# Kernel optimization log

Hardware: AMD Instinct MI355X
Metric: run time of the kernel (lower is better)

The kernel has to match this reference:

```python
import jax, jax.numpy as jnp
import numpy as np

ALPHA = 0.2  # LeakyReLU slope
BN_EPS = 1e-5


def _conv_circ(x, w, b, pad_w):
    # circular padding only on width (torch padding=(0, pad_w), padding_mode='circular')
    x = jnp.pad(x, ((0, 0), (0, 0), (0, 0), (pad_w, pad_w)), mode='wrap')
    y = jax.lax.conv_general_dilated(x, w, window_strides=(1, 1), padding='VALID',
                                     dimension_numbers=('NCHW', 'OIHW', 'NCHW'))
    return y + b[None, :, None, None]


def _graph_conv(x, n, w, b, pad_w):
    h1 = _conv_circ(x, w, b, pad_w)  # [B, N, C, F]
    h2 = _conv_circ(n, w, b, pad_w)
    B, N, C, F = h1.shape
    h1f = h1.reshape(B, N, C * F)
    h2f = h2.reshape(B, N, C * F)
    a = jnp.einsum('bnf,bmf->bnm', h1f, h2f)          # [B, N, N]
    a = jnp.where(a > 0, a, ALPHA * a)                 # LeakyReLU
    att = jax.nn.softmax(a, axis=1)                    # torch Softmax(dim=1)
    return (att @ h1f).reshape(B, N, C, F)


def _bn_pool_relu(x, gamma, beta, mean, var):
    # eval-mode BatchNorm2d -> MaxPool2d((1,2)) -> ReLU
    inv = gamma / jnp.sqrt(var + BN_EPS)
    x = x * inv[None, :, None, None] + (beta - mean * inv)[None, :, None, None]
    W = x.shape[-1]
    W2 = (W // 2) * 2
    x = x[..., :W2].reshape(*x.shape[:-1], W2 // 2, 2).max(axis=-1)
    return jax.nn.relu(x)


def setup_inputs() -> dict:
    key = jax.random.key(0)
    ks = jax.random.split(key, 16)
    B = 16384
    return {
        'x': jax.random.normal(ks[0], (B, 5, 5, 50), jnp.float32),
        'conv1_w': jax.random.normal(ks[1], (32, 5, 5, 11), jnp.float32) * 0.1,
        'conv1_b': jax.random.normal(ks[2], (32,), jnp.float32) * 0.1,
        'bn1_gamma': jax.random.uniform(ks[3], (32,), jnp.float32, 0.5, 1.5),
        'bn1_beta': jax.random.normal(ks[4], (32,), jnp.float32) * 0.1,
        'bn1_mean': jax.random.normal(ks[5], (32,), jnp.float32) * 0.1,
        'bn1_var': jax.random.uniform(ks[6], (32,), jnp.float32, 0.5, 1.5),
        'conv2_w': jax.random.normal(ks[7], (32, 32, 1, 5), jnp.float32) * 0.1,
        'conv2_b': jax.random.normal(ks[8], (32,), jnp.float32) * 0.1,
        'bn2_gamma': jax.random.uniform(ks[9], (32,), jnp.float32, 0.5, 1.5),
        'bn2_beta': jax.random.normal(ks[10], (32,), jnp.float32) * 0.1,
        'bn2_mean': jax.random.normal(ks[11], (32,), jnp.float32) * 0.1,
        'bn2_var': jax.random.uniform(ks[12], (32,), jnp.float32, 0.5, 1.5),
        'lin_w': jax.random.normal(ks[13], (13, 384), jnp.float32) * 0.05,
        'lin_b': jax.random.normal(ks[14], (13,), jnp.float32) * 0.05,
    }


def reference(x, conv1_w, conv1_b, bn1_gamma, bn1_beta, bn1_mean, bn1_var,
              conv2_w, conv2_b, bn2_gamma, bn2_beta, bn2_mean, bn2_var,
              lin_w, lin_b):
    W = x.shape[-1]
    xa, na = x[..., :W // 2], x[..., W // 2:]
    xa = _graph_conv(xa, xa, conv1_w, conv1_b, 5)
    na = _graph_conv(na, na, conv1_w, conv1_b, 5)
    xa = _bn_pool_relu(xa, bn1_gamma, bn1_beta, bn1_mean, bn1_var)
    na = _bn_pool_relu(na, bn1_gamma, bn1_beta, bn1_mean, bn1_var)
    x2 = _graph_conv(xa, na, conv2_w, conv2_b, 2)
    n2 = _graph_conv(na, xa, conv2_w, conv2_b, 2)
    x2 = _bn_pool_relu(x2, bn2_gamma, bn2_beta, bn2_mean, bn2_var)
    n2 = _bn_pool_relu(n2, bn2_gamma, bn2_beta, bn2_mean, bn2_var)
    flat = jnp.concatenate([x2, n2], axis=-1).reshape(x.shape[0], -1)  # [B, 384]
    # Dropout(0.2) is identity in eval mode
    return flat @ lin_w.T + lin_b
```

## Files before the change

### kernel.cpp

```cpp
#include <hip/hip_runtime.h>
#include <math.h>

#define ALPHA 0.2f
#define BN_EPS 1e-5f

typedef __attribute__((ext_vector_type(8))) short short8;
typedef __attribute__((ext_vector_type(4))) float v4f;

__device__ __forceinline__ unsigned short f2bf_rne(float f) {
    union { float f; unsigned u; } x; x.f = f;
    unsigned r = x.u + 0x7FFFu + ((x.u >> 16) & 1u);
    return (unsigned short)(r >> 16);
}
__device__ __forceinline__ float bf2f(unsigned short h) {
    union { float f; unsigned u; } x; x.u = ((unsigned)h) << 16;
    return x.f;
}

__global__ __launch_bounds__(256) void prep_kernel(const float* __restrict__ w1,
                                                   const float* __restrict__ w2,
                                                   unsigned short* __restrict__ ws16) {
    int s = blockIdx.x * 256 + threadIdx.x;
    if (s < 1664) {
        int lane = s & 63;
        int ktnt = s >> 6;
        int Kt = ktnt % 13;
        int Nt = ktnt / 13;
        int oc = Nt * 16 + (lane & 15);
        int quad = lane >> 4;
        for (int j = 0; j < 8; ++j) {
            int kp = Kt * 32 + quad * 8 + j;
            int kw = kp & 15, ickh = kp >> 4;
            float w = 0.f;
            if (kw < 11 && ickh < 25) w = w1[oc * 275 + ickh * 11 + kw];
            unsigned short h = f2bf_rne(w);
            ws16[s * 8 + j] = h;
            ws16[13312 + s * 8 + j] = f2bf_rne(w - bf2f(h));
        }
    } else if (s < 2304) {
        int s2 = s - 1664;
        int lane = s2 & 63;
        int ktnt = s2 >> 6;
        int kw = ktnt >> 1;
        int nt = ktnt & 1;
        int oc = nt * 16 + (lane & 15);
        int quad = lane >> 4;
        for (int j = 0; j < 8; ++j) {
            int ic = quad * 8 + j;
            float w = w2[oc * 160 + ic * 5 + kw];
            unsigned short h = f2bf_rne(w);
            ws16[26624 + s2 * 8 + j] = h;
            ws16[31744 + s2 * 8 + j] = f2bf_rne(w - bf2f(h));
        }
    }
}

#define IT 4648
#define ATO 2112
#define P2O 4224
#define CSTO 9296
#define LDS_TOTAL (9296 + 128)
#define ABF_PER_IT 1844

__global__ __launch_bounds__(256, 4) void gcn_kernel(
    const float* __restrict__ x,
    const float* __restrict__ w1, const float* __restrict__ b1,
    const float* __restrict__ g1, const float* __restrict__ be1,
    const float* __restrict__ mu1, const float* __restrict__ va1,
    const float* __restrict__ w2, const float* __restrict__ b2,
    const float* __restrict__ g2, const float* __restrict__ be2,
    const float* __restrict__ mu2, const float* __restrict__ va2,
    const float* __restrict__ lw, const float* __restrict__ lb,
    const unsigned short* __restrict__ ws16,
    float* __restrict__ out)
{
    __shared__ float lds[LDS_TOTAL];
    float* cst = lds + CSTO;

    const int tid = threadIdx.x;
    const int b0  = blockIdx.x * 2;

    {
        const float2* xg2 = (const float2*)(x + (size_t)b0 * 1250);
        for (int i2 = tid; i2 < 1250; i2 += 256) {
            float2 v = xg2[i2];
            int i = 2 * i2;
            int it = (i >= 1250) ? 1 : 0;
            int j = i - it * 1250;
            int c = j / 250; int r = j - c * 250;
            int h = r / 50;  int w50 = r - h * 50;
            int ha = (w50 >= 25) ? 1 : 0;
            lds[it * IT + ((ha * 5 + c) * 5 + h) * 25 + (w50 - ha * 25)] = v.x;
            int w51 = w50 + 1;
            int hb = (w51 >= 25) ? 1 : 0;
            lds[it * IT + ((hb * 5 + c) * 5 + h) * 25 + (w51 - hb * 25)] = v.y;
        }
    }
    if (tid < 64) {
        int oc = tid & 31;
        if (tid < 32) {
            float inv = g1[oc] * rsqrtf(va1[oc] + BN_EPS);
            cst[oc]      = inv;
            cst[32 + oc] = be1[oc] - mu1[oc] * inv;
        } else {
            float inv = g2[oc] * rsqrtf(va2[oc] + BN_EPS);
            cst[64 + oc] = inv;
            cst[96 + oc] = be2[oc] - mu2[oc] * inv;
        }
    }
    __syncthreads();

    {
        unsigned* abf0 = (unsigned*)lds;
        for (int d = tid; d < 2 * ABF_PER_IT; d += 256) {
            int it = (d >= ABF_PER_IT) ? 1 : 0;
            int d2 = d - it * ABF_PER_IT;
            unsigned u = 0;
            if (d2 < 1800) {
                int R2 = d2 / 36, o = d2 - R2 * 36;
                int cp = (o >= 18) ? 1 : 0;
                int half = (R2 >= 25) ? 1 : 0;
                int ickh = R2 - half * 25;
                int e = 2 * o - (cp ? 37 : 0);
                const float* src = &lds[it * IT + (half * 25 + ickh) * 25];
                int p0 = e + 20; if (p0 >= 25) p0 -= 25; if (p0 >= 25) p0 -= 25;
                int p1 = e + 21; if (p1 >= 25) p1 -= 25; if (p1 >= 25) p1 -= 25;
                u = (unsigned)f2bf_rne(src[p0]) | ((unsigned)f2bf_rne(src[p1]) << 16);
            }
            abf0[it * IT + ATO + d2] = u;
        }
    }
    __syncthreads();

    {
        const int wave = tid >> 6, lane = tid & 63;
        const int it = wave >> 1;
        const int Mtb = (wave & 1) * 2;
        const int quad = lane >> 4, m16 = lane & 15;
        const int kw0 = (quad & 1) * 8;
        const int ickh0 = quad >> 1;
        const unsigned* abf = (const unsigned*)lds;

        int dwb[2];
#pragma unroll
        for (int mt = 0; mt < 2; ++mt) {
            int mg = (Mtb + mt) * 16 + m16;
            int half = (mg >= 25) ? 1 : 0;
            int pos = mg - half * 25; pos = (pos > 24) ? 24 : pos;
            int e0 = pos + kw0;
            int c = e0 & 1;
            int R2b = half * 25 + ickh0;
            dwb[mt] = it * IT + ATO + R2b * 36 + c * 18 + ((e0 + c) >> 1);
        }

        v4f zz = {0.f, 0.f, 0.f, 0.f};
        v4f acc[2][2];
        acc[0][0] = zz; acc[0][1] = zz; acc[1][0] = zz; acc[1][1] = zz;

        for (int Kt = 0; Kt < 13; ++Kt) {
            union { unsigned u[4]; short8 v; } af[2];
#pragma unroll
            for (int mt = 0; mt < 2; ++mt) {
                int base = dwb[mt] + Kt * 72;
                af[mt].u[0] = abf[base + 0];
                af[mt].u[1] = abf[base + 1];
                af[mt].u[2] = abf[base + 2];
                af[mt].u[3] = abf[base + 3];
            }
#pragma unroll
            for (int nt = 0; nt < 2; ++nt) {
                const short8* ph = (const short8*)(ws16 + ((nt * 13 + Kt) * 64 + lane) * 8);
                const short8* pl = (const short8*)(ws16 + 13312 + ((nt * 13 + Kt) * 64 + lane) * 8);
                short8 bh = *ph;
                short8 bl = *pl;
#pragma unroll
                for (int mt = 0; mt < 2; ++mt) {
                    acc[mt][nt] = __builtin_amdgcn_mfma_f32_16x16x32_bf16(af[mt].v, bh, acc[mt][nt], 0, 0, 0);
                    acc[mt][nt] = __builtin_amdgcn_mfma_f32_16x16x32_bf16(af[mt].v, bl, acc[mt][nt], 0, 0, 0);
                }
            }
        }

        float bias0 = b1[m16], bias1 = b1[16 + m16];
        unsigned short* U = (unsigned short*)(lds + it * IT);
#pragma unroll
        for (int mt = 0; mt < 2; ++mt) {
#pragma unroll
            for (int r = 0; r < 4; ++r) {
                int mg = (Mtb + mt) * 16 + quad * 4 + r;
                if (mg < 50) {
                    int half = (mg >= 25) ? 1 : 0;
                    int pos = mg - half * 25;
                    int kd = pos >> 1, par = pos & 1;
                    float v0 = acc[mt][0][r] + bias0;
                    float v1 = acc[mt][1][r] + bias1;
                    int ch0 = half * 32 + m16;
                    int ch1 = half * 32 + 16 + m16;
                    unsigned short h0 = f2bf_rne(v0);
                    unsigned short h1v = f2bf_rne(v1);
                    U[kd * 132 + ch0 * 2 + par] = h0;
                    U[2112 + kd * 132 + ch0 * 2 + par] = f2bf_rne(v0 - bf2f(h0));
                    U[kd * 132 + ch1 * 2 + par] = h1v;
                    U[2112 + kd * 132 + ch1 * 2 + par] = f2bf_rne(v1 - bf2f(h1v));
                }
            }
        }
    }
    __syncthreads();

    {
        const int wave = tid >> 6, lane = tid & 63;
        const int it = wave >> 1, half = wave & 1;
        const int m16 = lane & 15, q = lane >> 4;
        const unsigned* D = (const unsigned*)(lds + it * IT);
        short8 fh[2], fl[2];
#pragma unroll
        for (int t = 0; t < 2; ++t) {
            int row = half * 32 + t * 16 + m16;
            union { unsigned u[4]; short8 v; } H, L;
#pragma unroll
            for (int i = 0; i < 4; ++i) {
                int k0 = q * 8 + 2 * i;
                unsigned mh = D[(k0 >> 1) * 66 + row];
                unsigned ml = D[1056 + (k0 >> 1) * 66 + row];
                if (k0 == 24) { mh &= 0xFFFFu; ml &= 0xFFFFu; }
                if (k0 > 24)  { mh = 0u; ml = 0u; }
                H.u[i] = mh; L.u[i] = ml;
            }
            fh[t] = H.v; fl[t] = L.v;
        }
        v4f zz = {0.f, 0.f, 0.f, 0.f};
        v4f acc[2][2];
        acc[0][0] = zz; acc[0][1] = zz; acc[1][0] = zz; acc[1][1] = zz;
#pragma unroll
        for (int mt = 0; mt < 2; ++mt)
#pragma unroll
            for (int nt = 0; nt < 2; ++nt) {
                acc[mt][nt] = __builtin_amdgcn_mfma_f32_16x16x32_bf16(fh[mt], fh[nt], acc[mt][nt], 0, 0, 0);
                acc[mt][nt] = __builtin_amdgcn_mfma_f32_16x16x32_bf16(fh[mt], fl[nt], acc[mt][nt], 0, 0, 0);
                acc[mt][nt] = __builtin_amdgcn_mfma_f32_16x16x32_bf16(fl[mt], fh[nt], acc[mt][nt], 0, 0, 0);
            }
        float* A = &lds[it * IT + ATO];
#pragma unroll
        for (int mt = 0; mt < 2; ++mt)
#pragma unroll
            for (int nt = 0; nt < 2; ++nt)
#pragma unroll
                for (int r = 0; r < 4; ++r) {
                    int m = mt * 16 + q * 4 + r;
                    int n = nt * 16 + m16;
                    float s = acc[mt][nt][r];
                    s = (s > 0.f) ? s : ALPHA * s;
                    A[(half * 32 + m) * 33 + n] = s;
                }
    }
    __syncthreads();

    {
        int row = tid >> 1, q = tid & 1;
        int it = row >> 6, rm = row & 63;
        float* rp = &lds[it * IT + ATO + rm * 33];
        float ev[16];
        float mx = -INFINITY;
#pragma unroll
        for (int k = 0; k < 16; ++k) { ev[k] = rp[q + 2 * k]; mx = fmaxf(mx, ev[k]); }
        mx = fmaxf(mx, __shfl_xor(mx, 1));
        float s = 0.f;
#pragma unroll
        for (int k = 0; k < 16; ++k) { ev[k] = __expf(ev[k] - mx); s += ev[k]; }
        s += __shfl_xor(s, 1);
        float inv = 1.f / s;
#pragma unroll
        for (int k = 0; k < 16; ++k) rp[q + 2 * k] = ev[k] * inv;
    }
    __syncthreads();

    {
        const int wave = tid >> 6, lane = tid & 63;
        const int it = wave >> 1, half = wave & 1;
        const int m16 = lane & 15, q = lane >> 4;
        const unsigned short* U = (const unsigned short*)(lds + it * IT);
        const float* AT = &lds[it * IT + ATO];

        short8 ah[2], al[2];
#pragma unroll
        for (int mt = 0; mt < 2; ++mt) {
            int pos = mt * 16 + m16;
            int kd = pos >> 1, par = pos & 1;
            union { unsigned u[4]; short8 v; } H, L;
#pragma unroll
            for (int i = 0; i < 4; ++i) {
                int ch = half * 32 + q * 8 + 2 * i;
                unsigned h0 = U[kd * 132 + ch * 2 + par];
                unsigned h1u = U[kd * 132 + (ch + 1) * 2 + par];
                unsigned l0 = U[2112 + kd * 132 + ch * 2 + par];
                unsigned l1 = U[2112 + kd * 132 + (ch + 1) * 2 + par];
                H.u[i] = h0 | (h1u << 16);
                L.u[i] = l0 | (l1 << 16);
            }
            ah[mt] = H.v; al[mt] = L.v;
        }
        short8 bh[2], bl[2];
#pragma unroll
        for (int nt = 0; nt < 2; ++nt) {
            union { unsigned u[4]; short8 v; } H, L;
#pragma unroll
            for (int i = 0; i < 4; ++i) {
                unsigned hh = 0, ll = 0;
#pragma unroll
                for (int t = 0; t < 2; ++t) {
                    int m = q * 8 + 2 * i + t;
                    float a = AT[(half * 32 + m) * 33 + nt * 16 + m16];
                    unsigned short hx = f2bf_rne(a);
                    hh |= ((unsigned)hx) << (16 * t);
                    ll |= ((unsigned)f2bf_rne(a - bf2f(hx))) << (16 * t);
                }
                H.u[i] = hh; L.u[i] = ll;
            }
            bh[nt] = H.v; bl[nt] = L.v;
        }
        v4f zz = {0.f, 0.f, 0.f, 0.f};
        v4f acc[2][2];
        acc[0][0] = zz; acc[0][1] = zz; acc[1][0] = zz; acc[1][1] = zz;
#pragma unroll
        for (int mt = 0; mt < 2; ++mt)
#pragma unroll
            for (int nt = 0; nt < 2; ++nt) {
                acc[mt][nt] = __builtin_amdgcn_mfma_f32_16x16x32_bf16(ah[mt], bh[nt], acc[mt][nt], 0, 0, 0);
                acc[mt][nt] = __builtin_amdgcn_mfma_f32_16x16x32_bf16(ah[mt], bl[nt], acc[mt][nt], 0, 0, 0);
                acc[mt][nt] = __builtin_amdgcn_mfma_f32_16x16x32_bf16(al[mt], bh[nt], acc[mt][nt], 0, 0, 0);
            }

        __syncthreads();

        unsigned short* PT = (unsigned short*)(lds + it * IT) + half * 832;
#pragma unroll
        for (int mt = 0; mt < 2; ++mt)
#pragma unroll
            for (int nt = 0; nt < 2; ++nt) {
                int n = nt * 16 + m16;
                float inv = cst[n], sh = cst[32 + n];
#pragma unroll
                for (int rr = 0; rr < 2; ++rr) {
                    int pos0 = mt * 16 + q * 4 + rr * 2;
                    if (pos0 < 24) {
                        float v0 = acc[mt][nt][rr * 2] * inv + sh;
                        float v1 = acc[mt][nt][rr * 2 + 1] * inv + sh;
                        float p = fmaxf(fmaxf(v0, v1), 0.f);
                        int j = pos0 >> 1;
                        unsigned short h = f2bf_rne(p);
                        PT[(n >> 1) * 26 + j * 2 + (n & 1)] = h;
                        PT[416 + (n >> 1) * 26 + j * 2 + (n & 1)] = f2bf_rne(p - bf2f(h));
                    }
                }
            }
    }
    __syncthreads();

    {
        const int wave = tid >> 6, lane = tid & 63;
        const int it = wave >> 1, half = wave & 1;
        const int m16 = lane & 15, q = lane >> 4;
        const unsigned* PTD = (const unsigned*)(lds + it * IT) + half * 416;

        v4f zz = {0.f, 0.f, 0.f, 0.f};
        v4f acc[2]; acc[0] = zz; acc[1] = zz;
#pragma unroll
        for (int kw = 0; kw < 5; ++kw) {
            int owr = m16 + kw - 2;
            if (owr < 0) owr += 12;
            if (owr >= 12) owr -= 12;
            union { unsigned u[4]; short8 v; } H, L;
#pragma unroll
            for (int i = 0; i < 4; ++i) {
                H.u[i] = PTD[(q * 4 + i) * 13 + owr];
                L.u[i] = PTD[208 + (q * 4 + i) * 13 + owr];
            }
#pragma unroll
            for (int nt = 0; nt < 2; ++nt) {
                const short8* ph = (const short8*)(ws16 + 26624 + ((kw * 2 + nt) * 64 + lane) * 8);
                const short8* pl = (const short8*)(ws16 + 31744 + ((kw * 2 + nt) * 64 + lane) * 8);
                short8 wbh = *ph, wbl = *pl;
                acc[nt] = __builtin_amdgcn_mfma_f32_16x16x32_bf16(H.v, wbh, acc[nt], 0, 0, 0);
                acc[nt] = __builtin_amdgcn_mfma_f32_16x16x32_bf16(H.v, wbl, acc[nt], 0, 0, 0);
                acc[nt] = __builtin_amdgcn_mfma_f32_16x16x32_bf16(L.v, wbh, acc[nt], 0, 0, 0);
            }
        }
        if (q < 3) {
            unsigned* H2 = (unsigned*)(lds + it * IT) + 1056;
#pragma unroll
            for (int nt = 0; nt < 2; ++nt) {
                float bias = b2[nt * 16 + m16];
                int ch = half * 32 + nt * 16 + m16;
#pragma unroll
                for (int rr = 0; rr < 2; ++rr) {
                    float v0 = acc[nt][rr * 2] + bias;
                    float v1 = acc[nt][rr * 2 + 1] + bias;
                    unsigned short h0 = f2bf_rne(v0), h1u = f2bf_rne(v1);
                    H2[(q * 2 + rr) * 66 + ch] = (unsigned)h0 | ((unsigned)h1u << 16);
                    H2[528 + (q * 2 + rr) * 66 + ch] =
                        (unsigned)f2bf_rne(v0 - bf2f(h0)) |
                        ((unsigned)f2bf_rne(v1 - bf2f(h1u)) << 16);
                }
            }
        }
    }
    __syncthreads();

    {
        const int wave = tid >> 6, lane = tid & 63;
        const int it = wave >> 1, half = wave & 1;
        const int m16 = lane & 15, q = lane >> 4;
        const unsigned* D = (const unsigned*)(lds + it * IT) + 1056;
        short8 ah[2], al[2], bh[2], bl[2];
#pragma unroll
        for (int t = 0; t < 2; ++t) {
            int rowA = (1 - half) * 32 + t * 16 + m16;
            int rowB = half * 32 + t * 16 + m16;
            union { unsigned u[4]; short8 v; } HA, LA, HB, LB;
#pragma unroll
            for (int i = 0; i < 4; ++i) {
                int k0 = q * 8 + 2 * i;
                unsigned a_h = D[(k0 >> 1) * 66 + rowA];
                unsigned a_l = D[528 + (k0 >> 1) * 66 + rowA];
                unsigned b_h = D[(k0 >> 1) * 66 + rowB];
                unsigned b_l = D[528 + (k0 >> 1) * 66 + rowB];
                if (k0 > 10) { a_h = 0u; a_l = 0u; b_h = 0u; b_l = 0u; }
                HA.u[i] = a_h; LA.u[i] = a_l; HB.u[i] = b_h; LB.u[i] = b_l;
            }
            ah[t] = HA.v; al[t] = LA.v; bh[t] = HB.v; bl[t] = LB.v;
        }
        v4f zz = {0.f, 0.f, 0.f, 0.f};
        v4f acc[2][2];
        acc[0][0] = zz; acc[0][1] = zz; acc[1][0] = zz; acc[1][1] = zz;
#pragma unroll
        for (int mt = 0; mt < 2; ++mt)
#pragma unroll
            for (int nt = 0; nt < 2; ++nt) {
                acc[mt][nt] = __builtin_amdgcn_mfma_f32_16x16x32_bf16(ah[mt], bh[nt], acc[mt][nt], 0, 0, 0);
                acc[mt][nt] = __builtin_amdgcn_mfma_f32_16x16x32_bf16(ah[mt], bl[nt], acc[mt][nt], 0, 0, 0);
                acc[mt][nt] = __builtin_amdgcn_mfma_f32_16x16x32_bf16(al[mt], bh[nt], acc[mt][nt], 0, 0, 0);
            }
        float* A = &lds[it * IT + ATO];
#pragma unroll
        for (int mt = 0; mt < 2; ++mt)
#pragma unroll
            for (int nt = 0; nt < 2; ++nt)
#pragma unroll
                for (int r = 0; r < 4; ++r) {
                    int m = mt * 16 + q * 4 + r;
                    int n = nt * 16 + m16;
                    float s = acc[mt][nt][r];
                    s = (s > 0.f) ? s : ALPHA * s;
                    A[(half * 32 + m) * 33 + n] = s;
                }
    }
    __syncthreads();

    {
        int row = tid >> 1, q = tid & 1;
        int it = row >> 6, rm = row & 63;
        float* rp = &lds[it * IT + ATO + rm * 33];
        float ev[16];
        float mx = -INFINITY;
#pragma unroll
        for (int k = 0; k < 16; ++k) { ev[k] = rp[q + 2 * k]; mx = fmaxf(mx, ev[k]); }
        mx = fmaxf(mx, __shfl_xor(mx, 1));
        float s = 0.f;
#pragma unroll
        for (int k = 0; k < 16; ++k) { ev[k] = __expf(ev[k] - mx); s += ev[k]; }
        s += __shfl_xor(s, 1);
        float inv = 1.f / s;
#pragma unroll
        for (int k = 0; k < 16; ++k) rp[q + 2 * k] = ev[k] * inv;
    }
    __syncthreads();

    {
        const int wave = tid >> 6, lane = tid & 63;
        const int it = wave >> 1, half = wave & 1;
        const int m16 = lane & 15, q = lane >> 4;
        const unsigned short* U = (const unsigned short*)(lds + it * IT);
        const float* AT = &lds[it * IT + ATO];

        int kd = m16 >> 1, par = m16 & 1;
        union { unsigned u[4]; short8 v; } HA, LA;
#pragma unroll
        for (int i = 0; i < 4; ++i) {
            int ch = half * 32 + q * 8 + 2 * i;
            unsigned h0 = U[2112 + kd * 132 + ch * 2 + par];
            unsigned h1u = U[2112 + kd * 132 + (ch + 1) * 2 + par];
            unsigned l0 = U[3168 + kd * 132 + ch * 2 + par];
            unsigned l1 = U[3168 + kd * 132 + (ch + 1) * 2 + par];
            HA.u[i] = h0 | (h1u << 16);
            LA.u[i] = l0 | (l1 << 16);
        }
        short8 bh[2], bl[2];
#pragma unroll
        for (int nt = 0; nt < 2; ++nt) {
            union { unsigned u[4]; short8 v; } H, L;
#pragma unroll
            for (int i = 0; i < 4; ++i) {
                unsigned hh = 0, ll = 0;
#pragma unroll
                for (int t = 0; t < 2; ++t) {
                    int m = q * 8 + 2 * i + t;
                    float a = AT[(half * 32 + m) * 33 + nt * 16 + m16];
                    unsigned short hx = f2bf_rne(a);
                    hh |= ((unsigned)hx) << (16 * t);
                    ll |= ((unsigned)f2bf_rne(a - bf2f(hx))) << (16 * t);
                }
                H.u[i] = hh; L.u[i] = ll;
            }
            bh[nt] = H.v; bl[nt] = L.v;
        }
        v4f zz = {0.f, 0.f, 0.f, 0.f};
        v4f acc[2]; acc[0] = zz; acc[1] = zz;
#pragma unroll
        for (int nt = 0; nt < 2; ++nt) {
            acc[nt] = __builtin_amdgcn_mfma_f32_16x16x32_bf16(HA.v, bh[nt], acc[nt], 0, 0, 0);
            acc[nt] = __builtin_amdgcn_mfma_f32_16x16x32_bf16(HA.v, bl[nt], acc[nt], 0, 0, 0);
            acc[nt] = __builtin_amdgcn_mfma_f32_16x16x32_bf16(LA.v, bh[nt], acc[nt], 0, 0, 0);
        }
        if (q < 3) {
#pragma unroll
            for (int nt = 0; nt < 2; ++nt) {
                int n = nt * 16 + m16;
                float inv = cst[64 + n], sh = cst[96 + n];
#pragma unroll
                for (int rr = 0; rr < 2; ++rr) {
                    int j = q * 2 + rr;
                    float v0 = acc[nt][rr * 2] * inv + sh;
                    float v1 = acc[nt][rr * 2 + 1] * inv + sh;
                    lds[it * IT + P2O + n * 12 + half * 6 + j] =
                        fmaxf(fmaxf(v0, v1), 0.f);
                }
            }
        }
    }
    __syncthreads();

    if (tid < 208) {
        int s8 = tid & 7;
        int rest = tid >> 3;
        int it = (rest >= 13) ? 1 : 0;
        int o = rest - it * 13;
        const float4* wv4 = (const float4*)(lw + o * 384 + s8 * 48);
        const float4* fv4 = (const float4*)&lds[it * IT + P2O + s8 * 48];
        float s = 0.f;
#pragma unroll
        for (int i = 0; i < 12; ++i) {
            float4 w4 = wv4[i];
            float4 f4 = fv4[i];
            s += f4.x * w4.x + f4.y * w4.y + f4.z * w4.z + f4.w * w4.w;
        }
        s += __shfl_down(s, 4, 8);
        s += __shfl_down(s, 2, 8);
        s += __shfl_down(s, 1, 8);
        if (s8 == 0) out[(size_t)(b0 + it) * 13 + o] = s + lb[o];
    }
}

extern "C" void kernel_launch(void* const* d_in, const int* in_sizes, int n_in,
                              void* d_out, int out_size, void* d_ws, size_t ws_size,
                              hipStream_t stream) {
    const float* x   = (const float*)d_in[0];
    const float* w1  = (const float*)d_in[1];
    const float* b1  = (const float*)d_in[2];
    const float* g1  = (const float*)d_in[3];
    const float* be1 = (const float*)d_in[4];
    const float* mu1 = (const float*)d_in[5];
    const float* va1 = (const float*)d_in[6];
    const float* w2  = (const float*)d_in[7];
    const float* b2  = (const float*)d_in[8];
    const float* g2  = (const float*)d_in[9];
    const float* be2 = (const float*)d_in[10];
    const float* mu2 = (const float*)d_in[11];
    const float* va2 = (const float*)d_in[12];
    const float* lw  = (const float*)d_in[13];
    const float* lb  = (const float*)d_in[14];
    float* out = (float*)d_out;
    unsigned short* ws16 = (unsigned short*)d_ws;

    prep_kernel<<<9, 256, 0, stream>>>(w1, w2, ws16);

    int B = in_sizes[0] / 1250;
    gcn_kernel<<<B / 2, 256, 0, stream>>>(x, w1, b1, g1, be1, mu1, va1,
                                          w2, b2, g2, be2, mu2, va2, lw, lb,
                                          ws16, out);
}
```

Before: 304.7 us.

## Store input as padded bf16 rows and build MFMA operands via funnel shifts

The input tile is now converted to bf16 while loading and stored with circular padding already in place. The conv1 MFMA A-fragments are built directly from those padded rows using 64-bit funnel shifts, which removes the separate im2col repack pass and one barrier. The LDS layout is compacted, so occupancy is raised to 5 blocks per CU. The hi/lo bf16 split now uses the packed hardware convert instruction. The trade-offs are extra ALU work for the unaligned funnel loads and five dword reads per fragment instead of four, plus possible rounding differences from the hardware convert.

Result: faster. 290.3 us (-4.7%).

```diff
diff --git a/kernel.cpp b/kernel.cpp
--- a/kernel.cpp
+++ b/kernel.cpp
@@ -15,6 +15,20 @@
 __device__ __forceinline__ float bf2f(unsigned short h) {
     union { float f; unsigned u; } x; x.u = ((unsigned)h) << 16;
     return x.f;
+}
+__device__ __forceinline__ unsigned cvtpk_bf16(float a0, float a1) {
+    unsigned r;
+    asm("v_cvt_pk_bf16_f32 %0, %1, %2" : "=v"(r) : "v"(a0), "v"(a1));
+    return r;
+}
+__device__ __forceinline__ void hilo_pair(float a0, float a1, unsigned& hp, unsigned& lp) {
+    hp = cvtpk_bf16(a0, a1);
+    union { unsigned u; float f; } c0, c1;
+    c0.u = hp << 16; c1.u = hp & 0xFFFF0000u;
+    lp = cvtpk_bf16(a0 - c0.f, a1 - c1.f);
+}
+__device__ __forceinline__ unsigned funnel16(unsigned hi, unsigned lo, int sh) {
+    return (unsigned)((((unsigned long long)hi << 32) | lo) >> sh);
 }
 
 __global__ __launch_bounds__(256) void prep_kernel(const float* __restrict__ w1,
@@ -55,14 +69,13 @@
     }
 }
 
-#define IT 4648
-#define ATO 2112
-#define P2O 4224
-#define CSTO 9296
-#define LDS_TOTAL (9296 + 128)
-#define ABF_PER_IT 1844
-
-__global__ __launch_bounds__(256, 4) void gcn_kernel(
+#define IT 3848
+#define XBO 1716
+#define ATO 1716
+#define CSTO 7696
+#define LDS_TOTAL (7696 + 128)
+
+__global__ __launch_bounds__(256, 5) void gcn_kernel(
     const float* __restrict__ x,
     const float* __restrict__ w1, const float* __restrict__ b1,
     const float* __restrict__ g1, const float* __restrict__ be1,
@@ -87,13 +100,34 @@
             int i = 2 * i2;
             int it = (i >= 1250) ? 1 : 0;
             int j = i - it * 1250;
-            int c = j / 250; int r = j - c * 250;
-            int h = r / 50;  int w50 = r - h * 50;
-            int ha = (w50 >= 25) ? 1 : 0;
-            lds[it * IT + ((ha * 5 + c) * 5 + h) * 25 + (w50 - ha * 25)] = v.x;
-            int w51 = w50 + 1;
-            int hb = (w51 >= 25) ? 1 : 0;
-            lds[it * IT + ((hb * 5 + c) * 5 + h) * 25 + (w51 - hb * 25)] = v.y;
+            unsigned short* XU = (unsigned short*)(lds + it * IT + XBO);
+            {
+                int c = j / 250; int r = j - c * 250;
+                int h = r / 50;  int w50 = r - h * 50;
+                int ha = (w50 >= 25) ? 1 : 0;
+                int w = w50 - ha * 25;
+                int base = (ha * 25 + c * 5 + h) * 42;
+                unsigned short u = f2bf_rne(v.x);
+                XU[base + 5 + w] = u;
+                if (w >= 20) XU[base + w - 20] = u;
+                if (w <= 9)  XU[base + 30 + w] = u;
+            }
+            {
+                int j1 = j + 1;
+                int c = j1 / 250; int r = j1 - c * 250;
+                int h = r / 50;  int w51 = r - h * 50;
+                int hb = (w51 >= 25) ? 1 : 0;
+                int w = w51 - hb * 25;
+                int base = (hb * 25 + c * 5 + h) * 42;
+                unsigned short u = f2bf_rne(v.y);
+                XU[base + 5 + w] = u;
+                if (w >= 20) XU[base + w - 20] = u;
+                if (w <= 9)  XU[base + 30 + w] = u;
+            }
+        }
+        if (tid < 42) {
+            int itz = (tid >= 21) ? 1 : 0;
+            lds[itz * IT + XBO + 1050 + (tid - itz * 21)] = 0.f;
         }
     }
     if (tid < 64) {
@@ -111,46 +145,23 @@
     __syncthreads();
 
     {
-        unsigned* abf0 = (unsigned*)lds;
-        for (int d = tid; d < 2 * ABF_PER_IT; d += 256) {
-            int it = (d >= ABF_PER_IT) ? 1 : 0;
-            int d2 = d - it * ABF_PER_IT;
-            unsigned u = 0;
-            if (d2 < 1800) {
-                int R2 = d2 / 36, o = d2 - R2 * 36;
-                int cp = (o >= 18) ? 1 : 0;
-                int half = (R2 >= 25) ? 1 : 0;
-                int ickh = R2 - half * 25;
-                int e = 2 * o - (cp ? 37 : 0);
-                const float* src = &lds[it * IT + (half * 25 + ickh) * 25];
-                int p0 = e + 20; if (p0 >= 25) p0 -= 25; if (p0 >= 25) p0 -= 25;
-                int p1 = e + 21; if (p1 >= 25) p1 -= 25; if (p1 >= 25) p1 -= 25;
-                u = (unsigned)f2bf_rne(src[p0]) | ((unsigned)f2bf_rne(src[p1]) << 16);
-            }
-            abf0[it * IT + ATO + d2] = u;
-        }
-    }
-    __syncthreads();
-
-    {
         const int wave = tid >> 6, lane = tid & 63;
         const int it = wave >> 1;
         const int Mtb = (wave & 1) * 2;
         const int quad = lane >> 4, m16 = lane & 15;
         const int kw0 = (quad & 1) * 8;
         const int ickh0 = quad >> 1;
-        const unsigned* abf = (const unsigned*)lds;
-
-        int dwb[2];
+        const unsigned* XD = (const unsigned*)(lds + it * IT + XBO);
+
+        int ub[2], sh[2];
 #pragma unroll
         for (int mt = 0; mt < 2; ++mt) {
             int mg = (Mtb + mt) * 16 + m16;
             int half = (mg >= 25) ? 1 : 0;
             int pos = mg - half * 25; pos = (pos > 24) ? 24 : pos;
-            int e0 = pos + kw0;
-            int c = e0 & 1;
-            int R2b = half * 25 + ickh0;
-            dwb[mt] = it * IT + ATO + R2b * 36 + c * 18 + ((e0 + c) >> 1);
+            int ux = (half * 25 + ickh0) * 42 + pos + kw0;
+            ub[mt] = ux >> 1;
+            sh[mt] = (ux & 1) << 4;
         }
 
         v4f zz = {0.f, 0.f, 0.f, 0.f};
@@ -161,11 +172,13 @@
             union { unsigned u[4]; short8 v; } af[2];
 #pragma unroll
             for (int mt = 0; mt < 2; ++mt) {
-                int base = dwb[mt] + Kt * 72;
-                af[mt].u[0] = abf[base + 0];
-                af[mt].u[1] = abf[base + 1];
-                af[mt].u[2] = abf[base + 2];
-                af[mt].u[3] = abf[base + 3];
+                int b = ub[mt] + Kt * 42;
+                unsigned d0 = XD[b + 0], d1 = XD[b + 1], d2 = XD[b + 2];
+                unsigned d3 = XD[b + 3], d4 = XD[b + 4];
+                af[mt].u[0] = funnel16(d1, d0, sh[mt]);
+                af[mt].u[1] = funnel16(d2, d1, sh[mt]);
+                af[mt].u[2] = funnel16(d3, d2, sh[mt]);
+                af[mt].u[3] = funnel16(d4, d3, sh[mt]);
             }
 #pragma unroll
             for (int nt = 0; nt < 2; ++nt) {
@@ -199,9 +212,9 @@
                     unsigned short h0 = f2bf_rne(v0);
                     unsigned short h1v = f2bf_rne(v1);
                     U[kd * 132 + ch0 * 2 + par] = h0;
-                    U[2112 + kd * 132 + ch0 * 2 + par] = f2bf_rne(v0 - bf2f(h0));
+                    U[1716 + kd * 132 + ch0 * 2 + par] = f2bf_rne(v0 - bf2f(h0));
                     U[kd * 132 + ch1 * 2 + par] = h1v;
-                    U[2112 + kd * 132 + ch1 * 2 + par] = f2bf_rne(v1 - bf2f(h1v));
+                    U[1716 + kd * 132 + ch1 * 2 + par] = f2bf_rne(v1 - bf2f(h1v));
                 }
             }
         }
@@ -222,7 +235,7 @@
             for (int i = 0; i < 4; ++i) {
                 int k0 = q * 8 + 2 * i;
                 unsigned mh = D[(k0 >> 1) * 66 + row];
-                unsigned ml = D[1056 + (k0 >> 1) * 66 + row];
+                unsigned ml = D[858 + (k0 >> 1) * 66 + row];
                 if (k0 == 24) { mh &= 0xFFFFu; ml &= 0xFFFFu; }
                 if (k0 > 24)  { mh = 0u; ml = 0u; }
                 H.u[i] = mh; L.u[i] = ml;
@@ -293,8 +306,8 @@
                 int ch = half * 32 + q * 8 + 2 * i;
                 unsigned h0 = U[kd * 132 + ch * 2 + par];
                 unsigned h1u = U[kd * 132 + (ch + 1) * 2 + par];
-                unsigned l0 = U[2112 + kd * 132 + ch * 2 + par];
-                unsigned l1 = U[2112 + kd * 132 + (ch + 1) * 2 + par];
+                unsigned l0 = U[1716 + kd * 132 + ch * 2 + par];
+                unsigned l1 = U[1716 + kd * 132 + (ch + 1) * 2 + par];
                 H.u[i] = h0 | (h1u << 16);
                 L.u[i] = l0 | (l1 << 16);
             }
@@ -306,16 +319,12 @@
             union { unsigned u[4]; short8 v; } H, L;
 #pragma unroll
             for (int i = 0; i < 4; ++i) {
-                unsigned hh = 0, ll = 0;
-#pragma unroll
-                for (int t = 0; t < 2; ++t) {
-                    int m = q * 8 + 2 * i + t;
-                    float a = AT[(half * 32 + m) * 33 + nt * 16 + m16];
-                    unsigned short hx = f2bf_rne(a);
-                    hh |= ((unsigned)hx) << (16 * t);
-                    ll |= ((unsigned)f2bf_rne(a - bf2f(hx))) << (16 * t);
-                }
-                H.u[i] = hh; L.u[i] = ll;
+                int m = q * 8 + 2 * i;
+                float a0 = AT[(half * 32 + m) * 33 + nt * 16 + m16];
+                float a1 = AT[(half * 32 + m + 1) * 33 + nt * 16 + m16];
+                unsigned hp, lp;
+                hilo_pair(a0, a1, hp, lp);
+                H.u[i] = hp; L.u[i] = lp;
             }
             bh[nt] = H.v; bl[nt] = L.v;
         }
@@ -387,7 +396,7 @@
             }
         }
         if (q < 3) {
-            unsigned* H2 = (unsigned*)(lds + it * IT) + 1056;
+            unsigned* H2 = (unsigned*)(lds + it * IT) + 858;
 #pragma unroll
             for (int nt = 0; nt < 2; ++nt) {
                 float bias = b2[nt * 16 + m16];
@@ -396,11 +405,10 @@
                 for (int rr = 0; rr < 2; ++rr) {
                     float v0 = acc[nt][rr * 2] + bias;
                     float v1 = acc[nt][rr * 2 + 1] + bias;
-                    unsigned short h0 = f2bf_rne(v0), h1u = f2bf_rne(v1);
-                    H2[(q * 2 + rr) * 66 + ch] = (unsigned)h0 | ((unsigned)h1u << 16);
-                    H2[528 + (q * 2 + rr) * 66 + ch] =
-                        (unsigned)f2bf_rne(v0 - bf2f(h0)) |
-                        ((unsigned)f2bf_rne(v1 - bf2f(h1u)) << 16);
+                    unsigned hp, lp;
+                    hilo_pair(v0, v1, hp, lp);
+                    H2[(q * 2 + rr) * 66 + ch] = hp;
+                    H2[396 + (q * 2 + rr) * 66 + ch] = lp;
                 }
             }
         }
@@ -411,7 +419,7 @@
         const int wave = tid >> 6, lane = tid & 63;
         const int it = wave >> 1, half = wave & 1;
         const int m16 = lane & 15, q = lane >> 4;
-        const unsigned* D = (const unsigned*)(lds + it * IT) + 1056;
+        const unsigned* D = (const unsigned*)(lds + it * IT) + 858;
         short8 ah[2], al[2], bh[2], bl[2];
 #pragma unroll
         for (int t = 0; t < 2; ++t) {
@@ -422,9 +430,9 @@
             for (int i = 0; i < 4; ++i) {
                 int k0 = q * 8 + 2 * i;
                 unsigned a_h = D[(k0 >> 1) * 66 + rowA];
-                unsigned a_l = D[528 + (k0 >> 1) * 66 + rowA];
+                unsigned a_l = D[396 + (k0 >> 1) * 66 + rowA];
                 unsigned b_h = D[(k0 >> 1) * 66 + rowB];
-                unsigned b_l = D[528 + (k0 >> 1) * 66 + rowB];
+                unsigned b_l = D[396 + (k0 >> 1) * 66 + rowB];
                 if (k0 > 10) { a_h = 0u; a_l = 0u; b_h = 0u; b_l = 0u; }
                 HA.u[i] = a_h; LA.u[i] = a_l; HB.u[i] = b_h; LB.u[i] = b_l;
             }
@@ -488,10 +496,10 @@
 #pragma unroll
         for (int i = 0; i < 4; ++i) {
             int ch = half * 32 + q * 8 + 2 * i;
-            unsigned h0 = U[2112 + kd * 132 + ch * 2 + par];
-            unsigned h1u = U[2112 + kd * 132 + (ch + 1) * 2 + par];
-            unsigned l0 = U[3168 + kd * 132 + ch * 2 + par];
-            unsigned l1 = U[3168 + kd * 132 + (ch + 1) * 2 + par];
+            unsigned h0 = U[1716 + kd * 132 + ch * 2 + par];
+            unsigned h1u = U[1716 + kd * 132 + (ch + 1) * 2 + par];
+            unsigned l0 = U[2508 + kd * 132 + ch * 2 + par];
+            unsigned l1 = U[2508 + kd * 132 + (ch + 1) * 2 + par];
             HA.u[i] = h0 | (h1u << 16);
             LA.u[i] = l0 | (l1 << 16);
         }
@@ -501,16 +509,12 @@
             union { unsigned u[4]; short8 v; } H, L;
 #pragma unroll
             for (int i = 0; i < 4; ++i) {
-                unsigned hh = 0, ll = 0;
-#pragma unroll
-                for (int t = 0; t < 2; ++t) {
-                    int m = q * 8 + 2 * i + t;
-                    float a = AT[(half * 32 + m) * 33 + nt * 16 + m16];
-                    unsigned short hx = f2bf_rne(a);
-                    hh |= ((unsigned)hx) << (16 * t);
-                    ll |= ((unsigned)f2bf_rne(a - bf2f(hx))) << (16 * t);
-                }
-                H.u[i] = hh; L.u[i] = ll;
+                int m = q * 8 + 2 * i;
+                float a0 = AT[(half * 32 + m) * 33 + nt * 16 + m16];
+                float a1 = AT[(half * 32 + m + 1) * 33 + nt * 16 + m16];
+                unsigned hp, lp;
+                hilo_pair(a0, a1, hp, lp);
+                H.u[i] = hp; L.u[i] = lp;
             }
             bh[nt] = H.v; bl[nt] = L.v;
         }
@@ -532,7 +536,7 @@
                     int j = q * 2 + rr;
                     float v0 = acc[nt][rr * 2] * inv + sh;
                     float v1 = acc[nt][rr * 2 + 1] * inv + sh;
-                    lds[it * IT + P2O + n * 12 + half * 6 + j] =
+                    lds[it * IT + n * 12 + half * 6 + j] =
                         fmaxf(fmaxf(v0, v1), 0.f);
                 }
             }
@@ -546,7 +550,7 @@
         int it = (rest >= 13) ? 1 : 0;
         int o = rest - it * 13;
         const float4* wv4 = (const float4*)(lw + o * 384 + s8 * 48);
-        const float4* fv4 = (const float4*)&lds[it * IT + P2O + s8 * 48];
+        const float4* fv4 = (const float4*)&lds[it * IT + s8 * 48];
         float s = 0.f;
 #pragma unroll
         for (int i = 0; i < 12; ++i) {
```
